# Kernel tuning notes

Hardware: AMD Instinct MI355X
Metric: run time of the kernel (lower is better)

## Reference

```python
import jax, jax.numpy as jnp
import numpy as np


def setup_inputs() -> dict:
    key = jax.random.key(0)
    ks = jax.random.split(key, 7)
    B, C, H, W = 8, 512, 32, 32
    N = 4
    Cn = C // N
    return {
        "first": jax.random.normal(ks[0], (B, C, H, W), dtype=jnp.float32),
        "second": jax.random.normal(ks[1], (B, C, H, W), dtype=jnp.float32),
        "w1": jax.random.normal(ks[2], (Cn, Cn), dtype=jnp.float32) * 0.05,
        "w2": jax.random.normal(ks[3], (Cn, Cn), dtype=jnp.float32) * 0.05,
        "w3": jax.random.normal(ks[4], (Cn, Cn), dtype=jnp.float32) * 0.05,
        "w4": jax.random.normal(ks[5], (Cn, Cn), dtype=jnp.float32) * 0.05,
        "w5": jax.random.normal(ks[6], (C, N), dtype=jnp.float32) * 0.05,
        "head_count": N,
    }


def reference(first, second, w1, w2, w3, w4, w5, head_count):
    B, C, H, W = first.shape
    N = head_count
    Cn = C // N
    L = H * W
    f = first.reshape(B * N, Cn, L)   # [BN, Cn, L]
    s = second.reshape(B * N, Cn, L)
    # 1x1 convs (no bias) == channel matmuls
    key_t = jnp.einsum('oc,bcl->blo', w1, f)    # [BN, L, Cn]
    query = jnp.einsum('oc,bcl->bol', w2, s)    # [BN, Cn, L]
    scores = jnp.einsum('blc,bcm->blm', key_t, query)  # [BN, L, L]
    attn = jax.nn.softmax(scores, axis=2)
    v1_t = jnp.einsum('oc,bcl->blo', w3, f)     # [BN, L, Cn]
    v2 = jnp.einsum('oc,bcl->bol', w4, s)       # [BN, Cn, L]
    value = jnp.einsum('blc,bcm->blm', v1_t, v2)  # [BN, L, L]
    res = jnp.sum(attn * value, axis=2)         # [BN, L]
    res = res.reshape(B, N, H, W)
    out = jax.nn.relu(jnp.einsum('on,bnhw->bohw', w5, res))  # [B, C, H, W]
    return out
```

## Files before the change

### kernel.cpp

```cpp
#include <hip/hip_runtime.h>
#include <hip/hip_bf16.h>
#include <stdint.h>

constexpr int BN = 32;
constexpr int Cn = 128;
constexpr int L  = 1024;
constexpr int CC = 512;
constexpr int BB = 8;

typedef __bf16 bf16x8 __attribute__((ext_vector_type(8)));
typedef float  f32x4  __attribute__((ext_vector_type(4)));

__device__ inline unsigned short f2bf(float f) {
    unsigned int x = __float_as_uint(f);
    x += 0x7fffu + ((x >> 16) & 1u);
    return (unsigned short)(x >> 16);
}

__device__ inline void gl_lds16(const void* g, void* l) {
    typedef __attribute__((address_space(1))) const unsigned int GU;
    typedef __attribute__((address_space(3))) unsigned int LU;
    __builtin_amdgcn_global_load_lds((GU*)g, (LU*)l, 16, 0, 0);
}

__global__ __launch_bounds__(256)
void wsplit_kernel(const float* __restrict__ w1, const float* __restrict__ w2,
                   const float* __restrict__ w3, const float* __restrict__ w4,
                   unsigned short* __restrict__ whi, unsigned short* __restrict__ wlo)
{
    int idx = (blockIdx.x * 256 + threadIdx.x) * 4;
    int mat = idx >> 14;
    int off = idx & 16383;
    const float* w = (mat == 0) ? w1 : (mat == 1) ? w2 : (mat == 2) ? w3 : w4;
    float4 v = *(const float4*)&w[off];
    ushort4 hi, lo;
    hi.x = f2bf(v.x); lo.x = f2bf(v.x - __uint_as_float((unsigned)hi.x << 16));
    hi.y = f2bf(v.y); lo.y = f2bf(v.y - __uint_as_float((unsigned)hi.y << 16));
    hi.z = f2bf(v.z); lo.z = f2bf(v.z - __uint_as_float((unsigned)hi.z << 16));
    hi.w = f2bf(v.w); lo.w = f2bf(v.w - __uint_as_float((unsigned)hi.w << 16));
    *(ushort4*)&whi[idx] = hi;
    *(ushort4*)&wlo[idx] = lo;
}

__global__ __launch_bounds__(256, 2)
void proj_kernel(const float* __restrict__ first, const float* __restrict__ second,
                 const unsigned short* __restrict__ whi,
                 const unsigned short* __restrict__ wlo,
                 unsigned short* __restrict__ outP)
{
    __shared__ unsigned short xs[2][16384];

    const int p     = blockIdx.x;
    const int strip = p & 7;
    const int src   = (p >> 3) & 1;
    const int bn    = p >> 4;

    const float* x = (src == 0 ? first : second) + (size_t)bn * Cn * L + strip * 128;
    const int m0 = src;
    const int m1 = 2 + src;
    const unsigned short* WH[2] = { whi + m0 * 16384, whi + m1 * 16384 };
    const unsigned short* WL[2] = { wlo + m0 * 16384, wlo + m1 * 16384 };
    unsigned short* Pm[2] = { outP + (size_t)(m0 * BN + bn) * (L * Cn),
                              outP + (size_t)(m1 * BN + bn) * (L * Cn) };

    const int tid = threadIdx.x;

    {
        const int l  = tid & 127;
        const int ch = tid >> 7;
        #pragma unroll
        for (int i = 0; i < 16; ++i) {
            int q  = (i << 1) | ch;
            int c0 = q << 2;
            float v0 = x[(size_t)(c0 + 0) * L + l];
            float v1 = x[(size_t)(c0 + 1) * L + l];
            float v2 = x[(size_t)(c0 + 2) * L + l];
            float v3 = x[(size_t)(c0 + 3) * L + l];
            ushort4 hi, lo;
            hi.x = f2bf(v0); lo.x = f2bf(v0 - __uint_as_float((unsigned)hi.x << 16));
            hi.y = f2bf(v1); lo.y = f2bf(v1 - __uint_as_float((unsigned)hi.y << 16));
            hi.z = f2bf(v2); lo.z = f2bf(v2 - __uint_as_float((unsigned)hi.z << 16));
            hi.w = f2bf(v3); lo.w = f2bf(v3 - __uint_as_float((unsigned)hi.w << 16));
            int slot = (c0 >> 3) ^ (l & 15);
            int off  = l * 128 + slot * 8 + (c0 & 7);
            *(ushort4*)&xs[0][off] = hi;
            *(ushort4*)&xs[1][off] = lo;
        }
    }

    const int lane = tid & 63;
    const int wv   = tid >> 6;
    const int oh   = wv & 1;
    const int lh   = wv >> 1;
    const int r16  = lane & 15;
    const int g    = lane >> 4;

    f32x4 acc[2][4][4];
    #pragma unroll
    for (int m = 0; m < 2; ++m)
        #pragma unroll
        for (int a = 0; a < 4; ++a)
            #pragma unroll
            for (int b = 0; b < 4; ++b) acc[m][a][b] = (f32x4){0.f, 0.f, 0.f, 0.f};

    __syncthreads();

    #pragma unroll
    for (int kkp = 0; kkp < 2; ++kkp)
    #pragma unroll
    for (int ogp = 0; ogp < 2; ++ogp) {
        bf16x8 ah[2][2][2], al[2][2][2];
        #pragma unroll
        for (int mat = 0; mat < 2; ++mat)
            #pragma unroll
            for (int og2 = 0; og2 < 2; ++og2)
                #pragma unroll
                for (int kk2 = 0; kk2 < 2; ++kk2) {
                    int o = oh * 64 + (ogp * 2 + og2) * 16 + r16;
                    int c = (kkp * 2 + kk2) * 32 + g * 8;
                    ah[mat][og2][kk2] = *(const bf16x8*)&WH[mat][o * 128 + c];
                    al[mat][og2][kk2] = *(const bf16x8*)&WL[mat][o * 128 + c];
                }
        #pragma unroll
        for (int lg = 0; lg < 4; ++lg) {
            int l = lh * 64 + lg * 16 + r16;
            bf16x8 bh[2], bl[2];
            #pragma unroll
            for (int kk2 = 0; kk2 < 2; ++kk2) {
                int slot = ((kkp * 2 + kk2) * 4 + g) ^ (l & 15);
                bh[kk2] = *(const bf16x8*)&xs[0][l * 128 + slot * 8];
                bl[kk2] = *(const bf16x8*)&xs[1][l * 128 + slot * 8];
            }
            #pragma unroll
            for (int mat = 0; mat < 2; ++mat)
                #pragma unroll
                for (int og2 = 0; og2 < 2; ++og2) {
                    f32x4 a = acc[mat][ogp * 2 + og2][lg];
                    #pragma unroll
                    for (int kk2 = 0; kk2 < 2; ++kk2) {
                        a = __builtin_amdgcn_mfma_f32_16x16x32_bf16(ah[mat][og2][kk2], bh[kk2], a, 0, 0, 0);
                        a = __builtin_amdgcn_mfma_f32_16x16x32_bf16(al[mat][og2][kk2], bh[kk2], a, 0, 0, 0);
                        a = __builtin_amdgcn_mfma_f32_16x16x32_bf16(ah[mat][og2][kk2], bl[kk2], a, 0, 0, 0);
                    }
                    acc[mat][ogp * 2 + og2][lg] = a;
                }
        }
    }

    #pragma unroll
    for (int mat = 0; mat < 2; ++mat)
        #pragma unroll
        for (int og = 0; og < 4; ++og)
            #pragma unroll
            for (int lg = 0; lg < 4; ++lg) {
                int o0 = oh * 64 + og * 16 + g * 4;
                int l  = strip * 128 + lh * 64 + lg * 16 + r16;
                f32x4 a = acc[mat][og][lg];
                ushort4 st;
                st.x = f2bf(a.x); st.y = f2bf(a.y);
                st.z = f2bf(a.z); st.w = f2bf(a.w);
                int pos = (((o0 >> 3) ^ (l & 7)) << 3) | (o0 & 7);
                *(ushort4*)&Pm[mat][(size_t)l * 128 + pos] = st;
            }
}

__global__ __launch_bounds__(256, 2)
void attn_kernel(const unsigned short* __restrict__ Pb,
                 float* __restrict__ Dp, float* __restrict__ Rp)
{
    __shared__ char smem[2][2][16384];

    const int p   = blockIdx.x;
    const int xcd = p & 7;
    const int jj  = p >> 3;
    const int bn  = xcd * 4 + (jj & 3);
    const int lt  = (jj >> 2) & 7;
    const int mh  = jj >> 5;

    const int tid  = threadIdx.x;
    const int lane = tid & 63;
    const int w    = tid >> 6;
    const int r16  = lane & 15;
    const int g    = lane >> 4;
    const int swz  = lane & 7;

    const size_t slab = (size_t)L * Cn;
    const unsigned short* Kt  = Pb + (size_t)(0 * BN + bn) * slab;
    const unsigned short* Qt  = Pb + (size_t)(1 * BN + bn) * slab;
    const unsigned short* V1t = Pb + (size_t)(2 * BN + bn) * slab;
    const unsigned short* V2t = Pb + (size_t)(3 * BN + bn) * slab;

    const int lbase = lt * 128;

    bf16x8 ka[2][4], va[2][4];
    #pragma unroll
    for (int i = 0; i < 2; ++i)
        #pragma unroll
        for (int kk = 0; kk < 4; ++kk) {
            int row = lbase + w * 32 + i * 16 + r16;
            int cp = ((kk << 2) + g) ^ swz;
            ka[i][kk] = *(const bf16x8*)(Kt  + (size_t)row * 128 + cp * 8);
            va[i][kk] = *(const bf16x8*)(V1t + (size_t)row * 128 + cp * 8);
        }

    const f32x4 z = {0.f, 0.f, 0.f, 0.f};
    f32x4 Dv[2] = {z, z};
    f32x4 Rv[2] = {z, z};

    auto STAGE = [&](int buf, int t) {
        const int m0 = mh * 512 + t * 64;
        const char* qs = (const char*)Qt  + (size_t)m0 * 256;
        const char* vs = (const char*)V2t + (size_t)m0 * 256;
        char* qd = &smem[buf][0][0];
        char* vd = &smem[buf][1][0];
        #pragma unroll
        for (int it = 0; it < 4; ++it) {
            gl_lds16(qs + tid * 16 + it * 4096, qd + tid * 16 + it * 4096);
            gl_lds16(vs + tid * 16 + it * 4096, vd + tid * 16 + it * 4096);
        }
    };

    auto COMPUTE = [&](int buf) {
        const char* qb = &smem[buf][0][0];
        const char* vb = &smem[buf][1][0];
        #pragma unroll
        for (int cg = 0; cg < 4; ++cg) {
            const int brow = cg * 16 + r16;
            const int rbase = brow * 256;
            bf16x8 qf[4], vf[4];
            #pragma unroll
            for (int kk = 0; kk < 4; ++kk) {
                int off = rbase + ((((kk << 2) + g) ^ swz) << 4);
                qf[kk] = *(const bf16x8*)(qb + off);
                vf[kk] = *(const bf16x8*)(vb + off);
            }
            f32x4 s0 = z, s1 = z, u0 = z, u1 = z;
            #pragma unroll
            for (int kk = 0; kk < 4; ++kk) {
                s0 = __builtin_amdgcn_mfma_f32_16x16x32_bf16(ka[0][kk], qf[kk], s0, 0, 0, 0);
                s1 = __builtin_amdgcn_mfma_f32_16x16x32_bf16(ka[1][kk], qf[kk], s1, 0, 0, 0);
                u0 = __builtin_amdgcn_mfma_f32_16x16x32_bf16(va[0][kk], vf[kk], u0, 0, 0, 0);
                u1 = __builtin_amdgcn_mfma_f32_16x16x32_bf16(va[1][kk], vf[kk], u1, 0, 0, 0);
            }
            f32x4 e0, e1;
            e0.x = __expf(s0.x - 8.f); e0.y = __expf(s0.y - 8.f);
            e0.z = __expf(s0.z - 8.f); e0.w = __expf(s0.w - 8.f);
            e1.x = __expf(s1.x - 8.f); e1.y = __expf(s1.y - 8.f);
            e1.z = __expf(s1.z - 8.f); e1.w = __expf(s1.w - 8.f);
            Dv[0] += e0;      Dv[1] += e1;
            Rv[0] += e0 * u0; Rv[1] += e1 * u1;
        }
    };

    STAGE(0, 0);
    __syncthreads();
    for (int t = 0; t < 8; ++t) {
        if (t < 7) STAGE((t + 1) & 1, t + 1);
        COMPUTE(t & 1);
        __syncthreads();
    }

    #pragma unroll
    for (int off = 8; off >= 1; off >>= 1) {
        #pragma unroll
        for (int i = 0; i < 2; ++i) {
            #pragma unroll
            for (int r = 0; r < 4; ++r) {
                Dv[i][r] += __shfl_xor(Dv[i][r], off);
                Rv[i][r] += __shfl_xor(Rv[i][r], off);
            }
        }
    }
    if (r16 == 0) {
        #pragma unroll
        for (int i = 0; i < 2; ++i)
            #pragma unroll
            for (int r = 0; r < 4; ++r) {
                int l = lbase + w * 32 + i * 16 + g * 4 + r;
                size_t idx = (size_t)mh * BN * L + (size_t)bn * L + l;
                Dp[idx] = Dv[i][r];
                Rp[idx] = Rv[i][r];
            }
    }
}

__global__ __launch_bounds__(256)
void combine_kernel(const float* __restrict__ Dp, const float* __restrict__ Rp,
                    float* __restrict__ res)
{
    int i = blockIdx.x * 256 + threadIdx.x;
    float d = Dp[i] + Dp[BN * L + i];
    float r = Rp[i] + Rp[BN * L + i];
    res[i] = r / d;
}

__global__ __launch_bounds__(256)
void out_kernel(const float* __restrict__ res, const float* __restrict__ w5,
                float* __restrict__ out)
{
    const int blk = blockIdx.x;
    const int o = blk & 511;
    const int b = blk >> 9;
    const float4 wv = *(const float4*)&w5[o * 4];

    const float* r0 = res + (size_t)(b * 4 + 0) * L;
    const float* r1 = res + (size_t)(b * 4 + 1) * L;
    const float* r2 = res + (size_t)(b * 4 + 2) * L;
    const float* r3 = res + (size_t)(b * 4 + 3) * L;

    const int hw = threadIdx.x * 4;
    float4 a0 = *(const float4*)&r0[hw];
    float4 a1 = *(const float4*)&r1[hw];
    float4 a2 = *(const float4*)&r2[hw];
    float4 a3 = *(const float4*)&r3[hw];

    float4 ov;
    ov.x = fmaxf(0.f, wv.x * a0.x + wv.y * a1.x + wv.z * a2.x + wv.w * a3.x);
    ov.y = fmaxf(0.f, wv.x * a0.y + wv.y * a1.y + wv.z * a2.y + wv.w * a3.y);
    ov.z = fmaxf(0.f, wv.x * a0.z + wv.y * a1.z + wv.z * a2.z + wv.w * a3.z);
    ov.w = fmaxf(0.f, wv.x * a0.w + wv.y * a1.w + wv.z * a2.w + wv.w * a3.w);

    *(float4*)&out[(size_t)blk * 1024 + hw] = ov;
}

extern "C" void kernel_launch(void* const* d_in, const int* in_sizes, int n_in,
                              void* d_out, int out_size, void* d_ws, size_t ws_size,
                              hipStream_t stream)
{
    const float* first  = (const float*)d_in[0];
    const float* second = (const float*)d_in[1];
    const float* w1 = (const float*)d_in[2];
    const float* w2 = (const float*)d_in[3];
    const float* w3 = (const float*)d_in[4];
    const float* w4 = (const float*)d_in[5];
    const float* w5 = (const float*)d_in[6];
    float* out = (float*)d_out;

    const size_t projBytes = (size_t)4 * BN * L * Cn * sizeof(unsigned short);
    unsigned short* P = (unsigned short*)d_ws;
    float* Dp  = (float*)((char*)d_ws + projBytes);
    float* Rp  = Dp + 2 * BN * L;
    float* res = Rp + 2 * BN * L;
    unsigned short* whi = (unsigned short*)(res + BN * L);
    unsigned short* wlo = whi + 4 * 16384;

    wsplit_kernel<<<dim3(64), dim3(256), 0, stream>>>(w1, w2, w3, w4, whi, wlo);
    proj_kernel<<<dim3(512), dim3(256), 0, stream>>>(first, second, whi, wlo, P);
    attn_kernel<<<dim3(512), dim3(256), 0, stream>>>(P, Dp, Rp);
    combine_kernel<<<dim3(BN * L / 256), dim3(256), 0, stream>>>(Dp, Rp, res);
    out_kernel<<<dim3(BB * CC), dim3(256), 0, stream>>>(res, w5, out);
}
```

Baseline: 67.16 us.

## Halve projection tile width to 64 positions and restructure K loop

The projection kernel now handles 64 spatial positions per block instead of 128, which doubles the grid to 1024 blocks and halves shared memory and accumulator registers. The inner loop is rebuilt as a non-unrolled loop over four K chunks with a scheduling barrier, loading all four output groups of weights per chunk. The aim is better occupancy and lower register pressure in a stage that is likely latency-bound. In exchange, each block reloads the full weight matrices for half as much work, so global and L2 traffic for weights doubles.

```diff
diff --git a/kernel.cpp b/kernel.cpp
--- a/kernel.cpp
+++ b/kernel.cpp
@@ -48,14 +48,14 @@
                  const unsigned short* __restrict__ wlo,
                  unsigned short* __restrict__ outP)
 {
-    __shared__ unsigned short xs[2][16384];
+    __shared__ unsigned short xs[2][64 * 128];
 
     const int p     = blockIdx.x;
-    const int strip = p & 7;
-    const int src   = (p >> 3) & 1;
-    const int bn    = p >> 4;
-
-    const float* x = (src == 0 ? first : second) + (size_t)bn * Cn * L + strip * 128;
+    const int strip = p & 15;
+    const int src   = (p >> 4) & 1;
+    const int bn    = p >> 5;
+
+    const float* x = (src == 0 ? first : second) + (size_t)bn * Cn * L + strip * 64;
     const int m0 = src;
     const int m1 = 2 + src;
     const unsigned short* WH[2] = { whi + m0 * 16384, whi + m1 * 16384 };
@@ -66,12 +66,11 @@
     const int tid = threadIdx.x;
 
     {
-        const int l  = tid & 127;
-        const int ch = tid >> 7;
-        #pragma unroll
-        for (int i = 0; i < 16; ++i) {
-            int q  = (i << 1) | ch;
-            int c0 = q << 2;
+        const int l   = tid & 63;
+        const int grp = tid >> 6;
+        #pragma unroll
+        for (int i = 0; i < 8; ++i) {
+            int c0 = grp * 32 + i * 4;
             float v0 = x[(size_t)(c0 + 0) * L + l];
             float v1 = x[(size_t)(c0 + 1) * L + l];
             float v2 = x[(size_t)(c0 + 2) * L + l];
@@ -95,56 +94,49 @@
     const int r16  = lane & 15;
     const int g    = lane >> 4;
 
-    f32x4 acc[2][4][4];
+    f32x4 acc[2][4][2];
     #pragma unroll
     for (int m = 0; m < 2; ++m)
         #pragma unroll
         for (int a = 0; a < 4; ++a)
             #pragma unroll
-            for (int b = 0; b < 4; ++b) acc[m][a][b] = (f32x4){0.f, 0.f, 0.f, 0.f};
+            for (int b = 0; b < 2; ++b) acc[m][a][b] = (f32x4){0.f, 0.f, 0.f, 0.f};
 
     __syncthreads();
 
-    #pragma unroll
-    for (int kkp = 0; kkp < 2; ++kkp)
-    #pragma unroll
-    for (int ogp = 0; ogp < 2; ++ogp) {
-        bf16x8 ah[2][2][2], al[2][2][2];
+    #pragma unroll 1
+    for (int kk = 0; kk < 4; ++kk) {
+        __builtin_amdgcn_sched_barrier(0);
+        bf16x8 ah[2][4], al[2][4];
         #pragma unroll
         for (int mat = 0; mat < 2; ++mat)
             #pragma unroll
-            for (int og2 = 0; og2 < 2; ++og2)
+            for (int og = 0; og < 4; ++og) {
+                int o = oh * 64 + og * 16 + r16;
+                int c = kk * 32 + g * 8;
+                ah[mat][og] = *(const bf16x8*)&WH[mat][o * 128 + c];
+                al[mat][og] = *(const bf16x8*)&WL[mat][o * 128 + c];
+            }
+        bf16x8 bh[2], bl[2];
+        #pragma unroll
+        for (int lg = 0; lg < 2; ++lg) {
+            int l = lh * 32 + lg * 16 + r16;
+            int slot = ((kk << 2) + g) ^ (l & 15);
+            bh[lg] = *(const bf16x8*)&xs[0][l * 128 + slot * 8];
+            bl[lg] = *(const bf16x8*)&xs[1][l * 128 + slot * 8];
+        }
+        #pragma unroll
+        for (int mat = 0; mat < 2; ++mat)
+            #pragma unroll
+            for (int og = 0; og < 4; ++og)
                 #pragma unroll
-                for (int kk2 = 0; kk2 < 2; ++kk2) {
-                    int o = oh * 64 + (ogp * 2 + og2) * 16 + r16;
-                    int c = (kkp * 2 + kk2) * 32 + g * 8;
-                    ah[mat][og2][kk2] = *(const bf16x8*)&WH[mat][o * 128 + c];
-                    al[mat][og2][kk2] = *(const bf16x8*)&WL[mat][o * 128 + c];
+                for (int lg = 0; lg < 2; ++lg) {
+                    f32x4 a = acc[mat][og][lg];
+                    a = __builtin_amdgcn_mfma_f32_16x16x32_bf16(ah[mat][og], bh[lg], a, 0, 0, 0);
+                    a = __builtin_amdgcn_mfma_f32_16x16x32_bf16(al[mat][og], bh[lg], a, 0, 0, 0);
+                    a = __builtin_amdgcn_mfma_f32_16x16x32_bf16(ah[mat][og], bl[lg], a, 0, 0, 0);
+                    acc[mat][og][lg] = a;
                 }
-        #pragma unroll
-        for (int lg = 0; lg < 4; ++lg) {
-            int l = lh * 64 + lg * 16 + r16;
-            bf16x8 bh[2], bl[2];
-            #pragma unroll
-            for (int kk2 = 0; kk2 < 2; ++kk2) {
-                int slot = ((kkp * 2 + kk2) * 4 + g) ^ (l & 15);
-                bh[kk2] = *(const bf16x8*)&xs[0][l * 128 + slot * 8];
-                bl[kk2] = *(const bf16x8*)&xs[1][l * 128 + slot * 8];
-            }
-            #pragma unroll
-            for (int mat = 0; mat < 2; ++mat)
-                #pragma unroll
-                for (int og2 = 0; og2 < 2; ++og2) {
-                    f32x4 a = acc[mat][ogp * 2 + og2][lg];
-                    #pragma unroll
-                    for (int kk2 = 0; kk2 < 2; ++kk2) {
-                        a = __builtin_amdgcn_mfma_f32_16x16x32_bf16(ah[mat][og2][kk2], bh[kk2], a, 0, 0, 0);
-                        a = __builtin_amdgcn_mfma_f32_16x16x32_bf16(al[mat][og2][kk2], bh[kk2], a, 0, 0, 0);
-                        a = __builtin_amdgcn_mfma_f32_16x16x32_bf16(ah[mat][og2][kk2], bl[kk2], a, 0, 0, 0);
-                    }
-                    acc[mat][ogp * 2 + og2][lg] = a;
-                }
-        }
     }
 
     #pragma unroll
@@ -152,9 +144,9 @@
         #pragma unroll
         for (int og = 0; og < 4; ++og)
             #pragma unroll
-            for (int lg = 0; lg < 4; ++lg) {
+            for (int lg = 0; lg < 2; ++lg) {
                 int o0 = oh * 64 + og * 16 + g * 4;
-                int l  = strip * 128 + lh * 64 + lg * 16 + r16;
+                int l  = strip * 64 + lh * 32 + lg * 16 + r16;
                 f32x4 a = acc[mat][og][lg];
                 ushort4 st;
                 st.x = f2bf(a.x); st.y = f2bf(a.y);
@@ -345,7 +337,7 @@
     unsigned short* wlo = whi + 4 * 16384;
 
     wsplit_kernel<<<dim3(64), dim3(256), 0, stream>>>(w1, w2, w3, w4, whi, wlo);
-    proj_kernel<<<dim3(512), dim3(256), 0, stream>>>(first, second, whi, wlo, P);
+    proj_kernel<<<dim3(1024), dim3(256), 0, stream>>>(first, second, whi, wlo, P);
     attn_kernel<<<dim3(512), dim3(256), 0, stream>>>(P, Dp, Rp);
     combine_kernel<<<dim3(BN * L / 256), dim3(256), 0, stream>>>(Dp, Rp, res);
     out_kernel<<<dim3(BB * CC), dim3(256), 0, stream>>>(res, w5, out);
```

Result: slower. 82.04 us (+22.2%).
